# Kernel tuning notes

Hardware: AMD Instinct MI355X
Metric: run time of the kernel (lower is better)

Reference implementation:

```python
import jax, jax.numpy as jnp
import numpy as np


def _grid_sample_2d(plane, gx, gy):
    """Bilinear sample plane (C,H,W) at normalized coords gx,gy in [-1,1].
    align_corners=True convention (standard in tri-plane NeRF code).
    Returns (N, C)."""
    C, H, W = plane.shape
    ix = (gx + 1.0) * 0.5 * (W - 1)  # x indexes width
    iy = (gy + 1.0) * 0.5 * (H - 1)  # y indexes height
    x0f = jnp.floor(ix)
    y0f = jnp.floor(iy)
    wx = ix - x0f  # (N,)
    wy = iy - y0f
    x0 = jnp.clip(x0f.astype(jnp.int32), 0, W - 1)
    x1 = jnp.clip(x0 + 1, 0, W - 1)
    y0 = jnp.clip(y0f.astype(jnp.int32), 0, H - 1)
    y1 = jnp.clip(y0 + 1, 0, H - 1)
    flat = plane.reshape(C, H * W)

    def gather(yi, xi):  # -> (N, C)
        return jnp.take(flat, yi * W + xi, axis=1).T

    w00 = ((1 - wx) * (1 - wy))[:, None]
    w01 = (wx * (1 - wy))[:, None]
    w10 = ((1 - wx) * wy)[:, None]
    w11 = (wx * wy)[:, None]
    return (gather(y0, x0) * w00 + gather(y0, x1) * w01 +
            gather(y1, x0) * w10 + gather(y1, x1) * w11)


def setup_inputs() -> dict:
    key = jax.random.key(0)
    ks = jax.random.split(key, 7)
    N, C, H1, H2 = 2097152, 32, 256, 4
    res = (727, 314, 1300)
    pts = jax.random.uniform(ks[0], (N, 3), jnp.float32, minval=-1.0, maxval=1.0)
    s = 0.1  # small init like typical plane init
    plane_yx = jax.random.normal(ks[1], (C, res[1], res[0]), jnp.float32) * s
    plane_zx = jax.random.normal(ks[2], (C, res[2], res[0]), jnp.float32) * s
    plane_zy = jax.random.normal(ks[3], (C, res[2], res[1]), jnp.float32) * s
    w1 = jax.random.normal(ks[4], (C, H1), jnp.float32) * (1.0 / np.sqrt(C))
    b1 = jnp.zeros((H1,), jnp.float32)
    w2 = jax.random.normal(ks[5], (H1, H2), jnp.float32) * (1.0 / np.sqrt(H1))
    b2 = jnp.zeros((H2,), jnp.float32)
    return {"pts": pts, "plane_yx": plane_yx, "plane_zx": plane_zx,
            "plane_zy": plane_zy, "w1": w1, "b1": b1, "w2": w2, "b2": b2}


def reference(pts, plane_yx, plane_zx, plane_zy, w1, b1, w2, b2):
    # tri-plane feature fetch: pairs (x,y), (x,z), (y,z)
    f_yx = _grid_sample_2d(plane_yx, pts[:, 0], pts[:, 1])  # (N, C)
    f_zx = _grid_sample_2d(plane_zx, pts[:, 0], pts[:, 2])
    f_zy = _grid_sample_2d(plane_zy, pts[:, 1], pts[:, 2])
    features = f_yx * f_zx * f_zy  # elementwise product over planes
    h = jax.nn.relu(features @ w1 + b1)  # decoder MLP
    out = h @ w2 + b2  # (N, out_dim)
    return out
```

## Files before the change

kernel.cpp:

```cpp
#include <hip/hip_runtime.h>
#include <hip/hip_fp16.h>
#include <hip/hip_bf16.h>

#define NC    32
#define NH1   256
#define W_YX  727
#define H_YX  314
#define W_ZX  727
#define H_ZX  1300
#define W_ZY  314
#define H_ZY  1300
#define HW_YX (W_YX * H_YX)
#define HW_ZX (W_ZX * H_ZX)
#define HW_ZY (W_ZY * H_ZY)

#define NBW1  32
#define NBW2  16
#define NB_YX ((HW_YX + 255) / 256)
#define NB_ZX ((HW_ZX + 255) / 256)
#define NB_ZY ((HW_ZY + 255) / 256)
#define NB_PREP (NBW1 + NBW2 + NB_YX + NB_ZX + NB_ZY)

#define PSTRIDE 12
#define FSTRIDE 20

typedef __attribute__((ext_vector_type(8))) short short8;
typedef __attribute__((ext_vector_type(4))) float f32x4;

__device__ __forceinline__ short f2bf(float f) {
    unsigned u = __float_as_uint(f);
    unsigned r = u + 0x7fffu + ((u >> 16) & 1u);
    return (short)(r >> 16);
}
__device__ __forceinline__ unsigned pk2(float a, float b) {
    union { __hip_bfloat162 h; unsigned u; } c;
    c.h = __float22bfloat162_rn(make_float2(a, b));
    return c.u;
}

__device__ __forceinline__ f32x4 ntload4(const float* p) {
    return __builtin_nontemporal_load((const f32x4*)p);
}
__device__ __forceinline__ float ntload1(const float* p) {
    return __builtin_nontemporal_load(p);
}

__device__ __forceinline__ void transpose_body(
    const float* __restrict__ src, unsigned short* __restrict__ dst,
    int HW, int hw0, int t)
{
    int c8 = t & 3;
    int r  = t >> 2;
    int hwt = hw0 + r * 4;

    if (hw0 + 256 <= HW) {
        f32x4 v[8];
#pragma unroll
        for (int cc = 0; cc < 8; ++cc) {
            int c = c8 * 8 + cc;
            v[cc] = ntload4(src + (size_t)c * HW + hwt);
        }
#pragma unroll
        for (int k = 0; k < 4; ++k) {
            uint4 o;
            unsigned* ou = &o.x;
#pragma unroll
            for (int e = 0; e < 4; ++e)
                ou[e] = pk2(v[2 * e][k], v[2 * e + 1][k]);
            *(uint4*)(dst + (size_t)(hwt + k) * NC + c8 * 8) = o;
        }
    } else {
        for (int k = 0; k < 4; ++k) {
            int hw = hwt + k;
            if (hw < HW) {
                uint4 o;
                unsigned* ou = &o.x;
#pragma unroll
                for (int e = 0; e < 4; ++e) {
                    float a = src[(size_t)(c8 * 8 + 2 * e) * HW + hw];
                    float b = src[(size_t)(c8 * 8 + 2 * e + 1) * HW + hw];
                    ou[e] = pk2(a, b);
                }
                *(uint4*)(dst + (size_t)hw * NC + c8 * 8) = o;
            }
        }
    }
}

__global__ __launch_bounds__(256) void kplane_prep_all(
    const float* __restrict__ pyx, const float* __restrict__ pzx,
    const float* __restrict__ pzy,
    const float* __restrict__ w1, const float* __restrict__ w2,
    unsigned short* __restrict__ tyx, unsigned short* __restrict__ tzx,
    unsigned short* __restrict__ tzy,
    short* __restrict__ w1a, short* __restrict__ w2a)
{
    int b = blockIdx.x;
    int t = threadIdx.x;

    if (b < NBW1) {
        int idx = b * 256 + t;
        int j    = idx & 7;
        int lane = (idx >> 3) & 63;
        int nt   = idx >> 9;
        int ch  = (lane >> 4) * 8 + j;
        int hid = nt * 16 + (lane & 15);
        w1a[idx] = f2bf(w1[ch * NH1 + hid]);
        return;
    }
    b -= NBW1;
    if (b < NBW2) {
        int idx = b * 256 + t;
        int j    = idx & 7;
        int lane = (idx >> 3) & 63;
        int kk   = idx >> 9;
        int o    = lane & 15;
        int quad = lane >> 4;
        int hid  = (2 * kk + (j >> 2)) * 16 + quad * 4 + (j & 3);
        float v  = (o < 4) ? w2[hid * 4 + o] : 0.0f;
        w2a[idx] = f2bf(v);
        return;
    }
    b -= NBW2;
    const float* src; unsigned short* dst; int HW;
    if (b < NB_YX)              { src = pyx; dst = tyx; HW = HW_YX; }
    else if (b < NB_YX + NB_ZX) { b -= NB_YX; src = pzx; dst = tzx; HW = HW_ZX; }
    else                        { b -= NB_YX + NB_ZX; src = pzy; dst = tzy; HW = HW_ZY; }
    transpose_body(src, dst, HW, b * 256, t);
}

__device__ __forceinline__ void bilin3(
    float gx, float gy, int W, int H,
    unsigned& o0, unsigned& o1, float& wx, float& wy)
{
    float ix  = (gx + 1.0f) * 0.5f * (float)(W - 1);
    float iy  = (gy + 1.0f) * 0.5f * (float)(H - 1);
    float x0f = floorf(ix), y0f = floorf(iy);
    wx = ix - x0f; wy = iy - y0f;
    int x0 = (int)x0f; x0 = x0 < 0 ? 0 : (x0 > W_YX - 1 ? W - 1 : x0);
    x0 = x0 > W - 1 ? W - 1 : x0;
    int y0 = (int)y0f; y0 = y0 < 0 ? 0 : (y0 > H - 1 ? H - 1 : y0);
    int y1 = y0 + 1; if (y1 > H - 1) y1 = H - 1;
    o0 = (unsigned)(y0 * W + x0) * 64u;
    o1 = (unsigned)(y1 * W + x0) * 64u;
}

template <bool FIRST>
__device__ __forceinline__ void corner4(
    const uint4& A, const uint4& B, const uint4& C, const uint4& D,
    float wx, float wy, float F[8])
{
    float w00 = (1.0f - wx) * (1.0f - wy);
    float w01 = wx * (1.0f - wy);
    float w10 = (1.0f - wx) * wy;
    float w11 = wx * wy;
    const unsigned* ua = &A.x; const unsigned* ub = &B.x;
    const unsigned* uc = &C.x; const unsigned* ud = &D.x;
#pragma unroll
    for (int e = 0; e < 4; ++e) {
        float a0 = __uint_as_float(ua[e] << 16);
        float a1 = __uint_as_float(ua[e] & 0xffff0000u);
        float b0 = __uint_as_float(ub[e] << 16);
        float b1 = __uint_as_float(ub[e] & 0xffff0000u);
        float c0 = __uint_as_float(uc[e] << 16);
        float c1 = __uint_as_float(uc[e] & 0xffff0000u);
        float d0 = __uint_as_float(ud[e] << 16);
        float d1 = __uint_as_float(ud[e] & 0xffff0000u);
        float v0 = w00 * a0; v0 = fmaf(w01, b0, v0);
        v0 = fmaf(w10, c0, v0); v0 = fmaf(w11, d0, v0);
        float v1 = w00 * a1; v1 = fmaf(w01, b1, v1);
        v1 = fmaf(w10, c1, v1); v1 = fmaf(w11, d1, v1);
        if (FIRST) { F[2 * e] = v0; F[2 * e + 1] = v1; }
        else       { F[2 * e] *= v0; F[2 * e + 1] *= v1; }
    }
}

__global__ __launch_bounds__(256) void kplane_fused(
    const float* __restrict__ pts,
    const unsigned short* __restrict__ tyx,
    const unsigned short* __restrict__ tzx,
    const unsigned short* __restrict__ tzy,
    const short* __restrict__ w1a, const short* __restrict__ w2a,
    const float* __restrict__ b1, const float* __restrict__ b2,
    float* __restrict__ out)
{
    __shared__ unsigned parS[256 * PSTRIDE];
    __shared__ unsigned featS[256 * FSTRIDE];

    int t = threadIdx.x;
    int base = blockIdx.x * 256;

    {
        float px = ntload1(&pts[(size_t)(base + t) * 3 + 0]);
        float py = ntload1(&pts[(size_t)(base + t) * 3 + 1]);
        float pz = ntload1(&pts[(size_t)(base + t) * 3 + 2]);
        unsigned a0, a1, c0, c1, d0, d1;
        float awx, awy, cwx, cwy, dwx, dwy;
        bilin3(px, py, W_YX, H_YX, a0, a1, awx, awy);
        bilin3(px, pz, W_ZX, H_ZX, c0, c1, cwx, cwy);
        bilin3(py, pz, W_ZY, H_ZY, d0, d1, dwx, dwy);
        uint4* P = (uint4*)&parS[t * PSTRIDE];
        uint4 P0 = {a0, a1, c0, c1};
        uint4 P1 = {d0, d1, __float_as_uint(awx), __float_as_uint(awy)};
        uint4 P2 = {__float_as_uint(cwx), __float_as_uint(cwy),
                    __float_as_uint(dwx), __float_as_uint(dwy)};
        P[0] = P0; P[1] = P1; P[2] = P2;
    }
    __syncthreads();

    {
        int q = t >> 2, j = t & 3;
        int jx16 = j * 16;
        const char* Byx = (const char*)tyx;
        const char* Bzx = (const char*)tzx;
        const char* Bzy = (const char*)tzy;
#pragma unroll
        for (int r = 0; r < 4; ++r) {
            int p = r * 64 + q;
            const uint4* P = (const uint4*)&parS[p * PSTRIDE];
            uint4 P0 = P[0], P1 = P[1], P2 = P[2];
            float awx = __uint_as_float(P1.z), awy = __uint_as_float(P1.w);
            float cwx = __uint_as_float(P2.x), cwy = __uint_as_float(P2.y);
            float dwx = __uint_as_float(P2.z), dwy = __uint_as_float(P2.w);

            uint4 La = *(const uint4*)(Byx + P0.x + jx16);
            uint4 Lb = *(const uint4*)(Byx + P0.x + 64 + jx16);
            uint4 Lc = *(const uint4*)(Byx + P0.y + jx16);
            uint4 Ld = *(const uint4*)(Byx + P0.y + 64 + jx16);
            uint4 Ma = *(const uint4*)(Bzx + P0.z + jx16);
            uint4 Mb = *(const uint4*)(Bzx + P0.z + 64 + jx16);
            uint4 Mc = *(const uint4*)(Bzx + P0.w + jx16);
            uint4 Md = *(const uint4*)(Bzx + P0.w + 64 + jx16);
            uint4 Na = *(const uint4*)(Bzy + P1.x + jx16);
            uint4 Nb = *(const uint4*)(Bzy + P1.x + 64 + jx16);
            uint4 Nc = *(const uint4*)(Bzy + P1.y + jx16);
            uint4 Nd = *(const uint4*)(Bzy + P1.y + 64 + jx16);

            float F[8];
            corner4<true >(La, Lb, Lc, Ld, awx, awy, F);
            corner4<false>(Ma, Mb, Mc, Md, cwx, cwy, F);
            corner4<false>(Na, Nb, Nc, Nd, dwx, dwy, F);

            uint4 o;
            o.x = pk2(F[0], F[1]); o.y = pk2(F[2], F[3]);
            o.z = pk2(F[4], F[5]); o.w = pk2(F[6], F[7]);
            *(uint4*)&featS[p * FSTRIDE + j * 4] = o;
        }
    }
    __syncthreads();

    {
        int w = t >> 6, lane = t & 63;
        int quad = lane >> 4, l15 = lane & 15;
        const short8* W1A = (const short8*)w1a;
        const short8* W2A = (const short8*)w2a;
        const float4* B1v = (const float4*)b1;
        float b20 = b2[0], b21 = b2[1], b22 = b2[2], b23 = b2[3];

#pragma unroll
        for (int mt = 0; mt < 4; ++mt) {
            int pt = w * 64 + mt * 16 + l15;
            union { uint4 v; short8 s; } bf;
            bf.v = *(const uint4*)&featS[pt * FSTRIDE + quad * 4];

            f32x4 acc = {0.f, 0.f, 0.f, 0.f};
#pragma unroll
            for (int kk = 0; kk < 8; ++kk) {
                float4 be = B1v[(2 * kk) * 4 + quad];
                float4 bo = B1v[(2 * kk + 1) * 4 + quad];
                f32x4 ze = {be.x, be.y, be.z, be.w};
                f32x4 zo = {bo.x, bo.y, bo.z, bo.w};
                ze = __builtin_amdgcn_mfma_f32_16x16x32_bf16(
                         W1A[(2 * kk) * 64 + lane], bf.s, ze, 0, 0, 0);
                zo = __builtin_amdgcn_mfma_f32_16x16x32_bf16(
                         W1A[(2 * kk + 1) * 64 + lane], bf.s, zo, 0, 0, 0);
                union { unsigned u[4]; short8 s; } hb;
                hb.u[0] = pk2(fmaxf(ze[0], 0.f), fmaxf(ze[1], 0.f));
                hb.u[1] = pk2(fmaxf(ze[2], 0.f), fmaxf(ze[3], 0.f));
                hb.u[2] = pk2(fmaxf(zo[0], 0.f), fmaxf(zo[1], 0.f));
                hb.u[3] = pk2(fmaxf(zo[2], 0.f), fmaxf(zo[3], 0.f));
                acc = __builtin_amdgcn_mfma_f32_16x16x32_bf16(
                          W2A[kk * 64 + lane], hb.s, acc, 0, 0, 0);
            }
            if (quad == 0) {
                f32x4 o = {acc[0] + b20, acc[1] + b21, acc[2] + b22, acc[3] + b23};
                __builtin_nontemporal_store(
                    o, (f32x4*)out + (base + w * 64 + mt * 16 + l15));
            }
        }
    }
}

__device__ __forceinline__ void bilin_full(
    float gx, float gy, int W, int H,
    int& o00, int& o01, int& o10, int& o11,
    float& w00, float& w01, float& w10, float& w11)
{
    float ix  = (gx + 1.0f) * 0.5f * (float)(W - 1);
    float iy  = (gy + 1.0f) * 0.5f * (float)(H - 1);
    float x0f = floorf(ix), y0f = floorf(iy);
    float wx  = ix - x0f,   wy  = iy - y0f;
    int x0 = (int)x0f; x0 = x0 < 0 ? 0 : (x0 > W - 1 ? W - 1 : x0);
    int y0 = (int)y0f; y0 = y0 < 0 ? 0 : (y0 > H - 1 ? H - 1 : y0);
    int x1 = x0 + 1; if (x1 > W - 1) x1 = W - 1;
    int y1 = y0 + 1; if (y1 > H - 1) y1 = H - 1;
    o00 = y0 * W + x0; o01 = y0 * W + x1;
    o10 = y1 * W + x0; o11 = y1 * W + x1;
    w00 = (1.0f - wx) * (1.0f - wy);
    w01 = wx * (1.0f - wy);
    w10 = (1.0f - wx) * wy;
    w11 = wx * wy;
}

__global__ __launch_bounds__(256) void kplane_fused_direct(
    const float* __restrict__ pts,
    const float* __restrict__ pyx, const float* __restrict__ pzx,
    const float* __restrict__ pzy,
    const float* __restrict__ w1, const float* __restrict__ b1,
    const float* __restrict__ w2, const float* __restrict__ b2,
    float* __restrict__ out, int N)
{
    int i = blockIdx.x * blockDim.x + threadIdx.x;
    if (i >= N) return;
    float px = pts[(size_t)i * 3 + 0];
    float py = pts[(size_t)i * 3 + 1];
    float pz = pts[(size_t)i * 3 + 2];

    int a00, a01, a10, a11; float aw00, aw01, aw10, aw11;
    int c00, c01, c10, c11; float cw00, cw01, cw10, cw11;
    int d00, d01, d10, d11; float dw00, dw01, dw10, dw11;
    bilin_full(px, py, W_YX, H_YX, a00, a01, a10, a11, aw00, aw01, aw10, aw11);
    bilin_full(px, pz, W_ZX, H_ZX, c00, c01, c10, c11, cw00, cw01, cw10, cw11);
    bilin_full(py, pz, W_ZY, H_ZY, d00, d01, d10, d11, dw00, dw01, dw10, dw11);

    float feat[NC];
#pragma unroll 4
    for (int c = 0; c < NC; ++c) {
        const float* byx = pyx + (size_t)c * HW_YX;
        const float* bzx = pzx + (size_t)c * HW_ZX;
        const float* bzy = pzy + (size_t)c * HW_ZY;
        float fyx = aw00 * byx[a00] + aw01 * byx[a01] + aw10 * byx[a10] + aw11 * byx[a11];
        float fzx = cw00 * bzx[c00] + cw01 * bzx[c01] + cw10 * bzx[c10] + cw11 * bzx[c11];
        float fzy = dw00 * bzy[d00] + dw01 * bzy[d01] + dw10 * bzy[d10] + dw11 * bzy[d11];
        feat[c] = fyx * fzx * fzy;
    }
    float o0 = b2[0], o1 = b2[1], o2 = b2[2], o3 = b2[3];
#pragma unroll 4
    for (int k = 0; k < NH1; ++k) {
        float hk = b1[k];
#pragma unroll
        for (int c = 0; c < NC; ++c)
            hk = fmaf(feat[c], w1[c * NH1 + k], hk);
        hk = fmaxf(hk, 0.0f);
        o0 = fmaf(hk, w2[k * 4 + 0], o0);
        o1 = fmaf(hk, w2[k * 4 + 1], o1);
        o2 = fmaf(hk, w2[k * 4 + 2], o2);
        o3 = fmaf(hk, w2[k * 4 + 3], o3);
    }
    float4 o; o.x = o0; o.y = o1; o.z = o2; o.w = o3;
    reinterpret_cast<float4*>(out)[i] = o;
}

extern "C" void kernel_launch(void* const* d_in, const int* in_sizes, int n_in,
                              void* d_out, int out_size, void* d_ws, size_t ws_size,
                              hipStream_t stream)
{
    const float* pts = (const float*)d_in[0];
    const float* pyx = (const float*)d_in[1];
    const float* pzx = (const float*)d_in[2];
    const float* pzy = (const float*)d_in[3];
    const float* w1  = (const float*)d_in[4];
    const float* b1  = (const float*)d_in[5];
    const float* w2  = (const float*)d_in[6];
    const float* b2  = (const float*)d_in[7];
    float* out = (float*)d_out;

    int N = in_sizes[0] / 3;

    size_t planes_e = (size_t)(HW_YX + HW_ZX + HW_ZY) * NC;
    size_t need = (planes_e + 8192 + 4096) * sizeof(short) + 256;

    if (ws_size >= need && (N % 256) == 0) {
        unsigned short* tyx = (unsigned short*)d_ws;
        unsigned short* tzx = tyx + (size_t)HW_YX * NC;
        unsigned short* tzy = tzx + (size_t)HW_ZX * NC;
        short* w1a = (short*)(tzy + (size_t)HW_ZY * NC);
        short* w2a = w1a + 8192;
        kplane_prep_all<<<NB_PREP, 256, 0, stream>>>(pyx, pzx, pzy, w1, w2,
                                                     tyx, tzx, tzy, w1a, w2a);
        kplane_fused<<<N / 256, 256, 0, stream>>>(pts, tyx, tzx, tzy,
                                                  w1a, w2a, b1, b2, out);
    } else {
        int blocks = (N + 255) / 256;
        kplane_fused_direct<<<blocks, 256, 0, stream>>>(pts, pyx, pzx, pzy,
                                                        w1, b1, w2, b2, out, N);
    }
}
```

Before: 581.3 us.

## Bin points spatially by (x,z) before sampling to improve gather locality

Adds a histogram, scan and scatter pass that buckets the points into 512 bins over (x,z) and writes them to a sorted buffer with their original index. The fused kernel then processes points bin-group by bin-group, with groups assigned to blocks by blockIdx mod 8, and scatters outputs back by original index. The aim is to keep the plane gathers for concurrently resident blocks within a smaller region of each plane so they hit in cache. In exchange it adds extra passes over all points, global and shared atomics, a 16-byte-per-point workspace buffer, and scattered output writes. It also removes the nontemporal load and store hints and fixes the x clamp in bilin3.

```diff
diff --git a/kernel.cpp b/kernel.cpp
--- a/kernel.cpp
+++ b/kernel.cpp
@@ -19,7 +19,12 @@
 #define NB_YX ((HW_YX + 255) / 256)
 #define NB_ZX ((HW_ZX + 255) / 256)
 #define NB_ZY ((HW_ZY + 255) / 256)
-#define NB_PREP (NBW1 + NBW2 + NB_YX + NB_ZX + NB_ZY)
+#define NB_HIST 1024
+#define NB_PREP (NBW1 + NBW2 + NB_YX + NB_ZX + NB_ZY + NB_HIST)
+
+#define NXB   32
+#define NZB   16
+#define NBINS (NXB * NZB)
 
 #define PSTRIDE 12
 #define FSTRIDE 20
@@ -38,11 +43,10 @@
     return c.u;
 }
 
-__device__ __forceinline__ f32x4 ntload4(const float* p) {
-    return __builtin_nontemporal_load((const f32x4*)p);
-}
-__device__ __forceinline__ float ntload1(const float* p) {
-    return __builtin_nontemporal_load(p);
+__device__ __forceinline__ int binkey(float px, float pz) {
+    int xb = (int)((px + 1.0f) * 16.0f); xb = xb < 0 ? 0 : (xb > NXB - 1 ? NXB - 1 : xb);
+    int zb = (int)((pz + 1.0f) * 8.0f);  zb = zb < 0 ? 0 : (zb > NZB - 1 ? NZB - 1 : zb);
+    return zb * NXB + xb;
 }
 
 __device__ __forceinline__ void transpose_body(
@@ -58,7 +62,7 @@
 #pragma unroll
         for (int cc = 0; cc < 8; ++cc) {
             int c = c8 * 8 + cc;
-            v[cc] = ntload4(src + (size_t)c * HW + hwt);
+            v[cc] = *(const f32x4*)(src + (size_t)c * HW + hwt);
         }
 #pragma unroll
         for (int k = 0; k < 4; ++k) {
@@ -91,10 +95,13 @@
     const float* __restrict__ pyx, const float* __restrict__ pzx,
     const float* __restrict__ pzy,
     const float* __restrict__ w1, const float* __restrict__ w2,
+    const float* __restrict__ pts, int N,
     unsigned short* __restrict__ tyx, unsigned short* __restrict__ tzx,
     unsigned short* __restrict__ tzy,
-    short* __restrict__ w1a, short* __restrict__ w2a)
-{
+    short* __restrict__ w1a, short* __restrict__ w2a,
+    unsigned* __restrict__ gHist)
+{
+    __shared__ unsigned lh[NBINS];
     int b = blockIdx.x;
     int t = threadIdx.x;
 
@@ -122,11 +129,71 @@
         return;
     }
     b -= NBW2;
-    const float* src; unsigned short* dst; int HW;
-    if (b < NB_YX)              { src = pyx; dst = tyx; HW = HW_YX; }
-    else if (b < NB_YX + NB_ZX) { b -= NB_YX; src = pzx; dst = tzx; HW = HW_ZX; }
-    else                        { b -= NB_YX + NB_ZX; src = pzy; dst = tzy; HW = HW_ZY; }
-    transpose_body(src, dst, HW, b * 256, t);
+    if (b < NB_YX + NB_ZX + NB_ZY) {
+        const float* src; unsigned short* dst; int HW;
+        if (b < NB_YX)              { src = pyx; dst = tyx; HW = HW_YX; }
+        else if (b < NB_YX + NB_ZX) { b -= NB_YX; src = pzx; dst = tzx; HW = HW_ZX; }
+        else                        { b -= NB_YX + NB_ZX; src = pzy; dst = tzy; HW = HW_ZY; }
+        transpose_body(src, dst, HW, b * 256, t);
+        return;
+    }
+    b -= NB_YX + NB_ZX + NB_ZY;
+    lh[t] = 0; lh[t + 256] = 0;
+    __syncthreads();
+    for (int i = b * 256 + t; i < N; i += NB_HIST * 256) {
+        float px = pts[(size_t)i * 3 + 0];
+        float pz = pts[(size_t)i * 3 + 2];
+        atomicAdd(&lh[binkey(px, pz)], 1u);
+    }
+    __syncthreads();
+    if (lh[t])       atomicAdd(&gHist[t], lh[t]);
+    if (lh[t + 256]) atomicAdd(&gHist[t + 256], lh[t + 256]);
+}
+
+__global__ __launch_bounds__(256) void ksort_scan(
+    const unsigned* __restrict__ gHist,
+    unsigned* __restrict__ cursor, unsigned* __restrict__ gBase, int N)
+{
+    __shared__ unsigned h[NBINS], sup[64];
+    int t = threadIdx.x;
+    h[t] = gHist[t]; h[t + 256] = gHist[t + 256];
+    __syncthreads();
+    if (t < 64) {
+        unsigned s = 0;
+#pragma unroll
+        for (int k = 0; k < 8; ++k) s += h[t * 8 + k];
+        sup[t] = s;
+    }
+    __syncthreads();
+    if (t == 0) {
+        unsigned a = 0;
+        for (int k = 0; k < 64; ++k) { unsigned v = sup[k]; sup[k] = a; a += v; }
+    }
+    __syncthreads();
+    if (t < 64) {
+        unsigned a = sup[t];
+#pragma unroll
+        for (int k = 0; k < 8; ++k) { unsigned v = h[t * 8 + k]; h[t * 8 + k] = a; a += v; }
+    }
+    __syncthreads();
+    cursor[t] = h[t]; cursor[t + 256] = h[t + 256];
+    if (t < NZB) gBase[t] = h[t * NXB];
+    if (t == 0)  gBase[NZB] = (unsigned)N;
+}
+
+__global__ __launch_bounds__(256) void ksort_scatter(
+    const float* __restrict__ pts, int N,
+    unsigned* __restrict__ cursor, float4* __restrict__ sp)
+{
+    for (int i = blockIdx.x * 256 + threadIdx.x; i < N; i += gridDim.x * 256) {
+        float px = pts[(size_t)i * 3 + 0];
+        float py = pts[(size_t)i * 3 + 1];
+        float pz = pts[(size_t)i * 3 + 2];
+        int key = binkey(px, pz);
+        unsigned slot = atomicAdd(&cursor[key], 1u);
+        float4 o; o.x = px; o.y = py; o.z = pz; o.w = __uint_as_float((unsigned)i);
+        sp[slot] = o;
+    }
 }
 
 __device__ __forceinline__ void bilin3(
@@ -137,8 +204,7 @@
     float iy  = (gy + 1.0f) * 0.5f * (float)(H - 1);
     float x0f = floorf(ix), y0f = floorf(iy);
     wx = ix - x0f; wy = iy - y0f;
-    int x0 = (int)x0f; x0 = x0 < 0 ? 0 : (x0 > W_YX - 1 ? W - 1 : x0);
-    x0 = x0 > W - 1 ? W - 1 : x0;
+    int x0 = (int)x0f; x0 = x0 < 0 ? 0 : (x0 > W - 1 ? W - 1 : x0);
     int y0 = (int)y0f; y0 = y0 < 0 ? 0 : (y0 > H - 1 ? H - 1 : y0);
     int y1 = y0 + 1; if (y1 > H - 1) y1 = H - 1;
     o0 = (unsigned)(y0 * W + x0) * 64u;
@@ -176,7 +242,7 @@
 }
 
 __global__ __launch_bounds__(256) void kplane_fused(
-    const float* __restrict__ pts,
+    const float4* __restrict__ sp, const unsigned* __restrict__ gBase, int cap,
     const unsigned short* __restrict__ tyx,
     const unsigned short* __restrict__ tzx,
     const unsigned short* __restrict__ tzy,
@@ -186,106 +252,121 @@
 {
     __shared__ unsigned parS[256 * PSTRIDE];
     __shared__ unsigned featS[256 * FSTRIDE];
+    __shared__ unsigned idxS[256];
 
     int t = threadIdx.x;
-    int base = blockIdx.x * 256;
-
-    {
-        float px = ntload1(&pts[(size_t)(base + t) * 3 + 0]);
-        float py = ntload1(&pts[(size_t)(base + t) * 3 + 1]);
-        float pz = ntload1(&pts[(size_t)(base + t) * 3 + 2]);
-        unsigned a0, a1, c0, c1, d0, d1;
-        float awx, awy, cwx, cwy, dwx, dwy;
-        bilin3(px, py, W_YX, H_YX, a0, a1, awx, awy);
-        bilin3(px, pz, W_ZX, H_ZX, c0, c1, cwx, cwy);
-        bilin3(py, pz, W_ZY, H_ZY, d0, d1, dwx, dwy);
-        uint4* P = (uint4*)&parS[t * PSTRIDE];
-        uint4 P0 = {a0, a1, c0, c1};
-        uint4 P1 = {d0, d1, __float_as_uint(awx), __float_as_uint(awy)};
-        uint4 P2 = {__float_as_uint(cwx), __float_as_uint(cwy),
-                    __float_as_uint(dwx), __float_as_uint(dwy)};
-        P[0] = P0; P[1] = P1; P[2] = P2;
-    }
-    __syncthreads();
-
-    {
-        int q = t >> 2, j = t & 3;
-        int jx16 = j * 16;
-        const char* Byx = (const char*)tyx;
-        const char* Bzx = (const char*)tzx;
-        const char* Bzy = (const char*)tzy;
-#pragma unroll
-        for (int r = 0; r < 4; ++r) {
-            int p = r * 64 + q;
-            const uint4* P = (const uint4*)&parS[p * PSTRIDE];
-            uint4 P0 = P[0], P1 = P[1], P2 = P[2];
-            float awx = __uint_as_float(P1.z), awy = __uint_as_float(P1.w);
-            float cwx = __uint_as_float(P2.x), cwy = __uint_as_float(P2.y);
-            float dwx = __uint_as_float(P2.z), dwy = __uint_as_float(P2.w);
-
-            uint4 La = *(const uint4*)(Byx + P0.x + jx16);
-            uint4 Lb = *(const uint4*)(Byx + P0.x + 64 + jx16);
-            uint4 Lc = *(const uint4*)(Byx + P0.y + jx16);
-            uint4 Ld = *(const uint4*)(Byx + P0.y + 64 + jx16);
-            uint4 Ma = *(const uint4*)(Bzx + P0.z + jx16);
-            uint4 Mb = *(const uint4*)(Bzx + P0.z + 64 + jx16);
-            uint4 Mc = *(const uint4*)(Bzx + P0.w + jx16);
-            uint4 Md = *(const uint4*)(Bzx + P0.w + 64 + jx16);
-            uint4 Na = *(const uint4*)(Bzy + P1.x + jx16);
-            uint4 Nb = *(const uint4*)(Bzy + P1.x + 64 + jx16);
-            uint4 Nc = *(const uint4*)(Bzy + P1.y + jx16);
-            uint4 Nd = *(const uint4*)(Bzy + P1.y + 64 + jx16);
-
-            float F[8];
-            corner4<true >(La, Lb, Lc, Ld, awx, awy, F);
-            corner4<false>(Ma, Mb, Mc, Md, cwx, cwy, F);
-            corner4<false>(Na, Nb, Nc, Nd, dwx, dwy, F);
-
-            uint4 o;
-            o.x = pk2(F[0], F[1]); o.y = pk2(F[2], F[3]);
-            o.z = pk2(F[4], F[5]); o.w = pk2(F[6], F[7]);
-            *(uint4*)&featS[p * FSTRIDE + j * 4] = o;
-        }
-    }
-    __syncthreads();
-
-    {
-        int w = t >> 6, lane = t & 63;
-        int quad = lane >> 4, l15 = lane & 15;
-        const short8* W1A = (const short8*)w1a;
-        const short8* W2A = (const short8*)w2a;
-        const float4* B1v = (const float4*)b1;
-        float b20 = b2[0], b21 = b2[1], b22 = b2[2], b23 = b2[3];
-
-#pragma unroll
-        for (int mt = 0; mt < 4; ++mt) {
-            int pt = w * 64 + mt * 16 + l15;
-            union { uint4 v; short8 s; } bf;
-            bf.v = *(const uint4*)&featS[pt * FSTRIDE + quad * 4];
-
-            f32x4 acc = {0.f, 0.f, 0.f, 0.f};
-#pragma unroll
-            for (int kk = 0; kk < 8; ++kk) {
-                float4 be = B1v[(2 * kk) * 4 + quad];
-                float4 bo = B1v[(2 * kk + 1) * 4 + quad];
-                f32x4 ze = {be.x, be.y, be.z, be.w};
-                f32x4 zo = {bo.x, bo.y, bo.z, bo.w};
-                ze = __builtin_amdgcn_mfma_f32_16x16x32_bf16(
-                         W1A[(2 * kk) * 64 + lane], bf.s, ze, 0, 0, 0);
-                zo = __builtin_amdgcn_mfma_f32_16x16x32_bf16(
-                         W1A[(2 * kk + 1) * 64 + lane], bf.s, zo, 0, 0, 0);
-                union { unsigned u[4]; short8 s; } hb;
-                hb.u[0] = pk2(fmaxf(ze[0], 0.f), fmaxf(ze[1], 0.f));
-                hb.u[1] = pk2(fmaxf(ze[2], 0.f), fmaxf(ze[3], 0.f));
-                hb.u[2] = pk2(fmaxf(zo[0], 0.f), fmaxf(zo[1], 0.f));
-                hb.u[3] = pk2(fmaxf(zo[2], 0.f), fmaxf(zo[3], 0.f));
-                acc = __builtin_amdgcn_mfma_f32_16x16x32_bf16(
-                          W2A[kk * 64 + lane], hb.s, acc, 0, 0, 0);
+    int bxcd = blockIdx.x & 7;
+    int i    = blockIdx.x >> 3;
+    int g    = bxcd + 8 * (i >= cap);
+    int j    = (i >= cap) ? i - cap : i;
+    unsigned gb = gBase[g], ge = gBase[g + 1];
+
+    for (unsigned start = gb + (unsigned)j * 256u; start < ge;
+         start += (unsigned)cap * 256u) {
+        int npts = (int)(ge - start); if (npts > 256) npts = 256;
+        __syncthreads();
+
+        {
+            uint4 P0 = {0,0,0,0}, P1 = {0,0,0,0}, P2 = {0,0,0,0};
+            unsigned oid = 0xFFFFFFFFu;
+            if (t < npts) {
+                float4 p = sp[start + t];
+                oid = __float_as_uint(p.w);
+                unsigned a0, a1, c0, c1, d0, d1;
+                float awx, awy, cwx, cwy, dwx, dwy;
+                bilin3(p.x, p.y, W_YX, H_YX, a0, a1, awx, awy);
+                bilin3(p.x, p.z, W_ZX, H_ZX, c0, c1, cwx, cwy);
+                bilin3(p.y, p.z, W_ZY, H_ZY, d0, d1, dwx, dwy);
+                P0 = {a0, a1, c0, c1};
+                P1 = {d0, d1, __float_as_uint(awx), __float_as_uint(awy)};
+                P2 = {__float_as_uint(cwx), __float_as_uint(cwy),
+                      __float_as_uint(dwx), __float_as_uint(dwy)};
             }
-            if (quad == 0) {
-                f32x4 o = {acc[0] + b20, acc[1] + b21, acc[2] + b22, acc[3] + b23};
-                __builtin_nontemporal_store(
-                    o, (f32x4*)out + (base + w * 64 + mt * 16 + l15));
+            uint4* P = (uint4*)&parS[t * PSTRIDE];
+            P[0] = P0; P[1] = P1; P[2] = P2;
+            idxS[t] = oid;
+        }
+        __syncthreads();
+
+        {
+            int q = t >> 2, jj = t & 3;
+            int jx16 = jj * 16;
+            const char* Byx = (const char*)tyx;
+            const char* Bzx = (const char*)tzx;
+            const char* Bzy = (const char*)tzy;
+#pragma unroll
+            for (int r = 0; r < 4; ++r) {
+                int p = r * 64 + q;
+                const uint4* P = (const uint4*)&parS[p * PSTRIDE];
+                uint4 P0 = P[0], P1 = P[1], P2 = P[2];
+                float awx = __uint_as_float(P1.z), awy = __uint_as_float(P1.w);
+                float cwx = __uint_as_float(P2.x), cwy = __uint_as_float(P2.y);
+                float dwx = __uint_as_float(P2.z), dwy = __uint_as_float(P2.w);
+
+                uint4 La = *(const uint4*)(Byx + P0.x + jx16);
+                uint4 Lb = *(const uint4*)(Byx + P0.x + 64 + jx16);
+                uint4 Lc = *(const uint4*)(Byx + P0.y + jx16);
+                uint4 Ld = *(const uint4*)(Byx + P0.y + 64 + jx16);
+                uint4 Ma = *(const uint4*)(Bzx + P0.z + jx16);
+                uint4 Mb = *(const uint4*)(Bzx + P0.z + 64 + jx16);
+                uint4 Mc = *(const uint4*)(Bzx + P0.w + jx16);
+                uint4 Md = *(const uint4*)(Bzx + P0.w + 64 + jx16);
+                uint4 Na = *(const uint4*)(Bzy + P1.x + jx16);
+                uint4 Nb = *(const uint4*)(Bzy + P1.x + 64 + jx16);
+                uint4 Nc = *(const uint4*)(Bzy + P1.y + jx16);
+                uint4 Nd = *(const uint4*)(Bzy + P1.y + 64 + jx16);
+
+                float F[8];
+                corner4<true >(La, Lb, Lc, Ld, awx, awy, F);
+                corner4<false>(Ma, Mb, Mc, Md, cwx, cwy, F);
+                corner4<false>(Na, Nb, Nc, Nd, dwx, dwy, F);
+
+                uint4 o;
+                o.x = pk2(F[0], F[1]); o.y = pk2(F[2], F[3]);
+                o.z = pk2(F[4], F[5]); o.w = pk2(F[6], F[7]);
+                *(uint4*)&featS[p * FSTRIDE + jj * 4] = o;
+            }
+        }
+        __syncthreads();
+
+        {
+            int w = t >> 6, lane = t & 63;
+            int quad = lane >> 4, l15 = lane & 15;
+            const short8* W1A = (const short8*)w1a;
+            const short8* W2A = (const short8*)w2a;
+            const float4* B1v = (const float4*)b1;
+            float b20 = b2[0], b21 = b2[1], b22 = b2[2], b23 = b2[3];
+
+#pragma unroll
+            for (int mt = 0; mt < 4; ++mt) {
+                int pt = w * 64 + mt * 16 + l15;
+                union { uint4 v; short8 s; } bf;
+                bf.v = *(const uint4*)&featS[pt * FSTRIDE + quad * 4];
+
+                f32x4 acc = {0.f, 0.f, 0.f, 0.f};
+#pragma unroll
+                for (int kk = 0; kk < 8; ++kk) {
+                    float4 be = B1v[(2 * kk) * 4 + quad];
+                    float4 bo = B1v[(2 * kk + 1) * 4 + quad];
+                    f32x4 ze = {be.x, be.y, be.z, be.w};
+                    f32x4 zo = {bo.x, bo.y, bo.z, bo.w};
+                    ze = __builtin_amdgcn_mfma_f32_16x16x32_bf16(
+                             W1A[(2 * kk) * 64 + lane], bf.s, ze, 0, 0, 0);
+                    zo = __builtin_amdgcn_mfma_f32_16x16x32_bf16(
+                             W1A[(2 * kk + 1) * 64 + lane], bf.s, zo, 0, 0, 0);
+                    union { unsigned u[4]; short8 s; } hb;
+                    hb.u[0] = pk2(fmaxf(ze[0], 0.f), fmaxf(ze[1], 0.f));
+                    hb.u[1] = pk2(fmaxf(ze[2], 0.f), fmaxf(ze[3], 0.f));
+                    hb.u[2] = pk2(fmaxf(zo[0], 0.f), fmaxf(zo[1], 0.f));
+                    hb.u[3] = pk2(fmaxf(zo[2], 0.f), fmaxf(zo[3], 0.f));
+                    acc = __builtin_amdgcn_mfma_f32_16x16x32_bf16(
+                              W2A[kk * 64 + lane], hb.s, acc, 0, 0, 0);
+                }
+                unsigned orig = idxS[pt];
+                if (quad == 0 && orig != 0xFFFFFFFFu) {
+                    f32x4 o = {acc[0] + b20, acc[1] + b21, acc[2] + b22, acc[3] + b23};
+                    *((f32x4*)out + orig) = o;
+                }
             }
         }
     }
@@ -377,19 +458,34 @@
 
     int N = in_sizes[0] / 3;
 
-    size_t planes_e = (size_t)(HW_YX + HW_ZX + HW_ZY) * NC;
-    size_t need = (planes_e + 8192 + 4096) * sizeof(short) + 256;
-
-    if (ws_size >= need && (N % 256) == 0) {
+    size_t planes_b = (size_t)(HW_YX + HW_ZX + HW_ZY) * NC * sizeof(short);
+    size_t frag_b   = (8192 + 4096) * sizeof(short);
+    size_t sort_b   = (size_t)N * 16;
+    size_t meta_b   = (NBINS + NBINS + 32) * sizeof(unsigned);
+    size_t need     = planes_b + frag_b + sort_b + meta_b + 256;
+
+    if (ws_size >= need) {
         unsigned short* tyx = (unsigned short*)d_ws;
         unsigned short* tzx = tyx + (size_t)HW_YX * NC;
         unsigned short* tzy = tzx + (size_t)HW_ZX * NC;
         short* w1a = (short*)(tzy + (size_t)HW_ZY * NC);
         short* w2a = w1a + 8192;
+        float4* sorted = (float4*)(w2a + 4096);
+        unsigned* gHist  = (unsigned*)(sorted + N);
+        unsigned* cursor = gHist + NBINS;
+        unsigned* gBase  = cursor + NBINS;
+
+        hipMemsetAsync(gHist, 0, NBINS * sizeof(unsigned), stream);
         kplane_prep_all<<<NB_PREP, 256, 0, stream>>>(pyx, pzx, pzy, w1, w2,
-                                                     tyx, tzx, tzy, w1a, w2a);
-        kplane_fused<<<N / 256, 256, 0, stream>>>(pts, tyx, tzx, tzy,
-                                                  w1a, w2a, b1, b2, out);
+                                                     pts, N, tyx, tzx, tzy,
+                                                     w1a, w2a, gHist);
+        ksort_scan<<<1, 256, 0, stream>>>(gHist, cursor, gBase, N);
+        ksort_scatter<<<2048, 256, 0, stream>>>(pts, N, cursor, sorted);
+
+        int cap = (N / NZB + N / (NZB * 4)) / 256 + 2;
+        kplane_fused<<<16 * cap, 256, 0, stream>>>(sorted, gBase, cap,
+                                                   tyx, tzx, tzy,
+                                                   w1a, w2a, b1, b2, out);
     } else {
         int blocks = (N + 255) / 256;
         kplane_fused_direct<<<blocks, 256, 0, stream>>>(pts, pyx, pzx, pzy,
```

New measurement: 1.227 ms. +111.1%, slower.
